# Optimization experiments

Measured on AMD Instinct MI355X. Metric: run time of the kernel, lower is better.

Reference implementation:

```python
import jax, jax.numpy as jnp
import numpy as np

B, T, C, H = 8, 2048, 1024, 128

def setup_inputs() -> dict:
    key = jax.random.key(0)
    kx, kq, kk, kv = jax.random.split(key, 4)
    x = jax.random.normal(kx, (B, T, C), dtype=jnp.float32)
    Wq = jax.random.normal(kq, (C, H), dtype=jnp.float32) * 0.02
    Wk = jax.random.normal(kk, (C, H), dtype=jnp.float32) * 0.02
    Wv = jax.random.normal(kv, (C, H), dtype=jnp.float32) * 0.02
    return {"x": x, "Wq": Wq, "Wk": Wk, "Wv": Wv}

def reference(x, Wq, Wk, Wv):
    # q,k,v: [B,T,H] via bias-free dense projections
    q = jnp.einsum('btc,ch->bth', x, Wq)
    k = jnp.einsum('btc,ch->bth', x, Wk)
    v = jnp.einsum('btc,ch->bth', x, Wv)
    scale = k.shape[-1] ** (-0.5)
    # scores: [B,T,T]
    wei = jnp.einsum('bth,bsh->bts', q, k) * scale
    Tlen = x.shape[1]
    causal = jnp.tril(jnp.ones((Tlen, Tlen), dtype=bool))  # True = keep
    wei = jnp.where(causal[None, :, :], wei, -jnp.inf)
    wei = jax.nn.softmax(wei, axis=-1)
    return jnp.einsum('bts,bsh->bth', wei, v)
```

## Files before the change

### kernel.cpp

```cpp
#include <hip/hip_runtime.h>

#define B_ 8
#define T_ 2048
#define C_ 1024
#define H_ 128
#define BT_ (B_*T_)

typedef unsigned short u16;
typedef unsigned int u32;
typedef __attribute__((ext_vector_type(4))) float f32x4;
typedef __attribute__((ext_vector_type(8))) __bf16 bf16x8;

__device__ __forceinline__ u16 f2bf(float f) {
  u32 u = __float_as_uint(f);
  u += 0x7fffu + ((u >> 16) & 1u);
  return (u16)(u >> 16);
}

#define GLL16(g, l) __builtin_amdgcn_global_load_lds( \
    (const __attribute__((address_space(1))) void*)(g), \
    (__attribute__((address_space(3))) void*)(l), 16, 0, 0)

__device__ __forceinline__ bf16x8 load_frag(const u16* base, int stride, int row0, int k0, int lane) {
  const u16* p = base + (size_t)(row0 + (lane & 15)) * stride + k0 + ((lane >> 4) << 3);
  return *reinterpret_cast<const bf16x8*>(p);
}

__device__ __forceinline__ bf16x8 cvt8n(f32x4 lo, f32x4 hi) {
  bf16x8 r;
#pragma unroll
  for (int i = 0; i < 4; i++) { r[i] = (__bf16)lo[i]; r[4 + i] = (__bf16)hi[i]; }
  return r;
}

__global__ void wt_kernel(const float* __restrict__ Wq, const float* __restrict__ Wk,
                          const float* __restrict__ Wv, u16* __restrict__ wt) {
  int mat = blockIdx.y;
  const float* W = (mat == 0) ? Wq : (mat == 1) ? Wk : Wv;
  int i = blockIdx.x * 256 + threadIdx.x;
  int h = i >> 10;
  int c = i & 1023;
  wt[mat * (C_ * H_) + i] = f2bf(W[c * H_ + h]);
}

__global__ __launch_bounds__(512, 4) void qkv_gemm(const float* __restrict__ x, const u16* __restrict__ wt,
                                                   u16* __restrict__ q, u16* __restrict__ k2,
                                                   u16* __restrict__ vt) {
  __shared__ __align__(16) float As[2][64 * 64];
  __shared__ __align__(16) u16 Bs[2][192 * 64];
  int t = threadIdx.x;
  int lane = t & 63, w = t >> 6;
  int wm = w >> 2, wn = w & 3;
  int quad = lane >> 4, col = lane & 15;
  int m0 = blockIdx.x * 64;
  int nb = blockIdx.y * 192;

  int arow = t >> 4;
  int acg = (t & 15) ^ (arow & 15);
  const float* ax0 = x + (size_t)(m0 + arow) * C_ + acg * 4;
  const float* ax1 = ax0 + (size_t)32 * C_;
  int brow = t >> 3;
  int bcg = (t & 7) ^ (brow & 7);
  const u16* bw0 = wt + (size_t)(nb + brow) * C_ + bcg * 8;
  const u16* bw1 = bw0 + (size_t)64 * C_;
  const u16* bw2 = bw0 + (size_t)128 * C_;

#define STAGE(st, buf) do { \
    int ko_ = (st) * 64; \
    GLL16(ax0 + ko_, &As[buf][t * 4]); \
    GLL16(ax1 + ko_, &As[buf][2048 + t * 4]); \
    GLL16(bw0 + ko_, &Bs[buf][t * 8]); \
    GLL16(bw1 + ko_, &Bs[buf][4096 + t * 8]); \
    GLL16(bw2 + ko_, &Bs[buf][8192 + t * 8]); \
  } while (0)

  STAGE(0, 0);

  f32x4 acc[2][3] = {};
#pragma unroll 2
  for (int kk = 0; kk < 16; kk++) {
    int cur = kk & 1;
    __syncthreads();
    if (kk + 1 < 16) STAGE(kk + 1, cur ^ 1);
    const float* Ab = &As[cur][0];
    const u16* Bb = &Bs[cur][0];
#pragma unroll
    for (int ks = 0; ks < 2; ks++) {
      bf16x8 af[2], bfr[3];
#pragma unroll
      for (int mt = 0; mt < 2; mt++) {
        int rr = wm * 32 + mt * 16 + col;
        int s0 = (ks * 8 + quad * 2) ^ (rr & 15);
        int s1 = s0 ^ 1;
        f32x4 lo = *reinterpret_cast<const f32x4*>(Ab + rr * 64 + s0 * 4);
        f32x4 hi = *reinterpret_cast<const f32x4*>(Ab + rr * 64 + s1 * 4);
        af[mt] = cvt8n(lo, hi);
      }
#pragma unroll
      for (int nt = 0; nt < 3; nt++) {
        int rr = wn * 48 + nt * 16 + col;
        int sl = (ks * 4 + quad) ^ (rr & 7);
        bfr[nt] = *reinterpret_cast<const bf16x8*>(Bb + rr * 64 + sl * 8);
      }
#pragma unroll
      for (int mt = 0; mt < 2; mt++)
#pragma unroll
        for (int nt = 0; nt < 3; nt++)
          acc[mt][nt] = __builtin_amdgcn_mfma_f32_16x16x32_bf16(af[mt], bfr[nt], acc[mt][nt], 0, 0, 0);
    }
  }
#undef STAGE

#pragma unroll
  for (int mt = 0; mt < 2; mt++) {
    int row0 = m0 + wm * 32 + mt * 16 + quad * 4;
#pragma unroll
    for (int nt = 0; nt < 3; nt++) {
      int n = nb + wn * 48 + nt * 16 + col;
      int mat = n >> 7, h = n & 127;
      if (mat == 0) {
#pragma unroll
        for (int r = 0; r < 4; r++) q[(size_t)(row0 + r) * H_ + h] = f2bf(acc[mt][nt][r]);
      } else if (mat == 1) {
#pragma unroll
        for (int r = 0; r < 4; r++) k2[(size_t)(row0 + r) * H_ + h] = f2bf(acc[mt][nt][r]);
      } else {
        int bb = row0 >> 11, tt = row0 & 2047;
        ushort4 pk;
        pk.x = f2bf(acc[mt][nt][0]); pk.y = f2bf(acc[mt][nt][1]);
        pk.z = f2bf(acc[mt][nt][2]); pk.w = f2bf(acc[mt][nt][3]);
        *reinterpret_cast<ushort4*>(&vt[((size_t)bb * H_ + h) * T_ + tt]) = pk;
      }
    }
  }
}

__global__ __launch_bounds__(256) void attn_part(const u16* __restrict__ q, const u16* __restrict__ k,
                                                 const u16* __restrict__ vt,
                                                 float* __restrict__ Op, float* __restrict__ lsum) {
  __shared__ __align__(16) u16 Ks[2][32 * 136];
  __shared__ __align__(16) u16 Vs[2][128 * 40];
  __shared__ __align__(16) u16 P[4][2][16 * 40];
  int t = threadIdx.x;
  int lane = t & 63, w = t >> 6;
  int quad = lane >> 4, col = lane & 15;
  int bx = blockIdx.x;
  int qt = 31 - (bx >> 4);
  int s = (bx >> 3) & 1;
  int b = bx & 7;
  const float scale = 0.08838834764831845f;

  int nk = 2 * (qt + 1);
  int n0 = qt + 1;
  int it0 = s ? n0 : 0;
  int it1 = s ? nk : n0;

  int krow0 = t >> 4, ke = (t & 15) * 8;
  int krow1 = krow0 + 16;
  int vrow0 = t >> 2, ve = (t & 3) * 8;
  int vrow1 = vrow0 + 64;

  int qrow0 = b * T_ + qt * 64 + w * 16;
  bf16x8 qf[4];
#pragma unroll
  for (int ks = 0; ks < 4; ks++) qf[ks] = load_frag(q, H_, qrow0, ks * 32, lane);

  f32x4 o[8] = {};
  float l[4] = {0.f, 0.f, 0.f, 0.f};
  int myqrow = qt * 64 + w * 16 + quad * 4;

  {
    const u16* kb = k + (size_t)(b * T_ + it0 * 32) * H_;
    *reinterpret_cast<uint4*>(&Ks[0][krow0 * 136 + ke]) = *reinterpret_cast<const uint4*>(kb + (size_t)krow0 * 128 + ke);
    *reinterpret_cast<uint4*>(&Ks[0][krow1 * 136 + ke]) = *reinterpret_cast<const uint4*>(kb + (size_t)krow1 * 128 + ke);
    const u16* vb = vt + (size_t)b * H_ * T_ + it0 * 32;
    *reinterpret_cast<uint4*>(&Vs[0][vrow0 * 40 + ve]) = *reinterpret_cast<const uint4*>(vb + (size_t)vrow0 * T_ + ve);
    *reinterpret_cast<uint4*>(&Vs[0][vrow1 * 40 + ve]) = *reinterpret_cast<const uint4*>(vb + (size_t)vrow1 * T_ + ve);
  }

  for (int kt = it0; kt < it1; kt++) {
    int cur = (kt - it0) & 1;
    __syncthreads();
    bool more = (kt + 1 < it1);
    uint4 kc0, kc1, vc0, vc1;
    if (more) {
      const u16* kb = k + (size_t)(b * T_ + (kt + 1) * 32) * H_;
      kc0 = *reinterpret_cast<const uint4*>(kb + (size_t)krow0 * 128 + ke);
      kc1 = *reinterpret_cast<const uint4*>(kb + (size_t)krow1 * 128 + ke);
      const u16* vb = vt + (size_t)b * H_ * T_ + (kt + 1) * 32;
      vc0 = *reinterpret_cast<const uint4*>(vb + (size_t)vrow0 * T_ + ve);
      vc1 = *reinterpret_cast<const uint4*>(vb + (size_t)vrow1 * T_ + ve);
    }

    f32x4 s0 = {}, s1 = {};
#pragma unroll
    for (int ks = 0; ks < 4; ks++) {
      bf16x8 kb0 = *reinterpret_cast<const bf16x8*>(&Ks[cur][col * 136 + ks * 32 + quad * 8]);
      bf16x8 kb1 = *reinterpret_cast<const bf16x8*>(&Ks[cur][(col + 16) * 136 + ks * 32 + quad * 8]);
      s0 = __builtin_amdgcn_mfma_f32_16x16x32_bf16(qf[ks], kb0, s0, 0, 0, 0);
      s1 = __builtin_amdgcn_mfma_f32_16x16x32_bf16(qf[ks], kb1, s1, 0, 0, 0);
    }

    float pv[8];
    int kcol0 = kt * 32 + col;
#pragma unroll
    for (int r = 0; r < 4; r++) {
      int qr = myqrow + r;
      float a0 = fminf(s0[r] * scale, 30.f);
      float a1 = fminf(s1[r] * scale, 30.f);
      a0 = (kcol0      > qr) ? -1e30f : a0;
      a1 = (kcol0 + 16 > qr) ? -1e30f : a1;
      float p0 = __expf(a0);
      float p1 = __expf(a1);
      pv[r] = p0; pv[4 + r] = p1;
      l[r] += p0 + p1;
    }

    u16* Pb = &P[w][cur][0];
#pragma unroll
    for (int r = 0; r < 4; r++) {
      Pb[(quad * 4 + r) * 40 + col] = f2bf(pv[r]);
      Pb[(quad * 4 + r) * 40 + col + 16] = f2bf(pv[4 + r]);
    }
    asm volatile("" ::: "memory");
    __builtin_amdgcn_s_waitcnt(0xc07f);
    asm volatile("" ::: "memory");
    bf16x8 pf = *reinterpret_cast<const bf16x8*>(&Pb[col * 40 + (quad << 3)]);

#pragma unroll
    for (int ht = 0; ht < 8; ht++) {
      bf16x8 vf = *reinterpret_cast<const bf16x8*>(&Vs[cur][(ht * 16 + col) * 40 + quad * 8]);
      o[ht] = __builtin_amdgcn_mfma_f32_16x16x32_bf16(pf, vf, o[ht], 0, 0, 0);
    }

    if (more) {
      int nxt = cur ^ 1;
      *reinterpret_cast<uint4*>(&Ks[nxt][krow0 * 136 + ke]) = kc0;
      *reinterpret_cast<uint4*>(&Ks[nxt][krow1 * 136 + ke]) = kc1;
      *reinterpret_cast<uint4*>(&Vs[nxt][vrow0 * 40 + ve]) = vc0;
      *reinterpret_cast<uint4*>(&Vs[nxt][vrow1 * 40 + ve]) = vc1;
    }
  }

#pragma unroll
  for (int r = 0; r < 4; r++) {
    float v = l[r];
    v += __shfl_xor(v, 1);
    v += __shfl_xor(v, 2);
    v += __shfl_xor(v, 4);
    v += __shfl_xor(v, 8);
    l[r] = v;
  }

  int tile = (s * 8 + b) * 32 + qt;
  float* Orow = Op + (size_t)tile * (64 * 128);
  float* lrow = lsum + (size_t)tile * 64;
  int rowin0 = w * 16 + quad * 4;
  if (col == 0) {
#pragma unroll
    for (int r = 0; r < 4; r++) lrow[rowin0 + r] = l[r];
  }
#pragma unroll
  for (int ht = 0; ht < 8; ht++) {
#pragma unroll
    for (int r = 0; r < 4; r++)
      Orow[(size_t)(rowin0 + r) * 128 + ht * 16 + col] = o[ht][r];
  }
}

__global__ __launch_bounds__(256) void attn_comb(const float* __restrict__ Op, const float* __restrict__ lsum,
                                                 float* __restrict__ out) {
  int bx = blockIdx.x;
  int b = bx >> 5, qt = bx & 31;
  int t = threadIdx.x;
  int h = t & 127, half = t >> 7;
  int tile0 = b * 32 + qt;
  int tile1 = tile0 + 256;
#pragma unroll 4
  for (int rr = 0; rr < 32; rr++) {
    int row = half * 32 + rr;
    float l0 = lsum[tile0 * 64 + row];
    float l1 = lsum[tile1 * 64 + row];
    float rl = 1.f / (l0 + l1);
    float v = (Op[(size_t)tile0 * 8192 + row * 128 + h] +
               Op[(size_t)tile1 * 8192 + row * 128 + h]) * rl;
    out[((size_t)(b * T_ + qt * 64 + row)) * H_ + h] = v;
  }
}

extern "C" void kernel_launch(void* const* d_in, const int* in_sizes, int n_in,
                              void* d_out, int out_size, void* d_ws, size_t ws_size,
                              hipStream_t stream) {
  (void)in_sizes; (void)n_in; (void)out_size; (void)ws_size;
  const float* x  = (const float*)d_in[0];
  const float* Wq = (const float*)d_in[1];
  const float* Wk = (const float*)d_in[2];
  const float* Wv = (const float*)d_in[3];
  u16* ws = (u16*)d_ws;
  u16* q  = ws;
  u16* k  = ws + (size_t)BT_ * H_;
  u16* vt = ws + 2 * (size_t)BT_ * H_;
  u16* wt = ws + 3 * (size_t)BT_ * H_;
  float* Op = (float*)(ws + 3 * (size_t)BT_ * H_ + 3 * C_ * H_);
  float* lsum = Op + (size_t)512 * 64 * 128;
  float* out = (float*)d_out;

  wt_kernel<<<dim3(512, 3), 256, 0, stream>>>(Wq, Wk, Wv, wt);
  qkv_gemm<<<dim3(BT_ / 64, 2), 512, 0, stream>>>(x, wt, q, k, vt);
  attn_part<<<dim3(512), 256, 0, stream>>>(q, k, vt, Op, lsum);
  attn_comb<<<dim3(256), 256, 0, stream>>>(Op, lsum, out);
}
```

Before: 162.3 us.

## Split attention KV range four ways and load K/V fragments directly from global

Attention partial kernel now splits each query tile's key range into four parts instead of two, doubling the grid to 1024 blocks. It drops the LDS double-buffering of K and V and instead loads MFMA fragments straight from global memory (relying on L2/cache), removing the block-wide barriers. The combine kernel now sums four partials. This trades LDS reuse across the four waves for more parallelism and fewer syncs, but each wave now redundantly fetches the same K/V from global memory, and the partial-output traffic doubles.

```diff
diff --git a/kernel.cpp b/kernel.cpp
--- a/kernel.cpp
+++ b/kernel.cpp
@@ -135,74 +135,59 @@
   }
 }
 
-__global__ __launch_bounds__(256) void attn_part(const u16* __restrict__ q, const u16* __restrict__ k,
-                                                 const u16* __restrict__ vt,
-                                                 float* __restrict__ Op, float* __restrict__ lsum) {
-  __shared__ __align__(16) u16 Ks[2][32 * 136];
-  __shared__ __align__(16) u16 Vs[2][128 * 40];
+__global__ __launch_bounds__(256, 4) void attn_part(const u16* __restrict__ q, const u16* __restrict__ k,
+                                                    const u16* __restrict__ vt,
+                                                    float* __restrict__ Op, float* __restrict__ lsum) {
   __shared__ __align__(16) u16 P[4][2][16 * 40];
   int t = threadIdx.x;
   int lane = t & 63, w = t >> 6;
   int quad = lane >> 4, col = lane & 15;
   int bx = blockIdx.x;
-  int qt = 31 - (bx >> 4);
-  int s = (bx >> 3) & 1;
+  int qt = 31 - (bx >> 5);
+  int s = (bx >> 3) & 3;
   int b = bx & 7;
   const float scale = 0.08838834764831845f;
 
   int nk = 2 * (qt + 1);
-  int n0 = qt + 1;
-  int it0 = s ? n0 : 0;
-  int it1 = s ? nk : n0;
-
-  int krow0 = t >> 4, ke = (t & 15) * 8;
-  int krow1 = krow0 + 16;
-  int vrow0 = t >> 2, ve = (t & 3) * 8;
-  int vrow1 = vrow0 + 64;
+  int it0 = (s * nk) >> 2;
+  int it1 = ((s + 1) * nk) >> 2;
 
   int qrow0 = b * T_ + qt * 64 + w * 16;
   bf16x8 qf[4];
 #pragma unroll
   for (int ks = 0; ks < 4; ks++) qf[ks] = load_frag(q, H_, qrow0, ks * 32, lane);
+
+  const u16* kb_b = k + (size_t)b * T_ * H_;
+  const u16* vb_b = vt + (size_t)b * H_ * T_;
 
   f32x4 o[8] = {};
   float l[4] = {0.f, 0.f, 0.f, 0.f};
   int myqrow = qt * 64 + w * 16 + quad * 4;
 
-  {
-    const u16* kb = k + (size_t)(b * T_ + it0 * 32) * H_;
-    *reinterpret_cast<uint4*>(&Ks[0][krow0 * 136 + ke]) = *reinterpret_cast<const uint4*>(kb + (size_t)krow0 * 128 + ke);
-    *reinterpret_cast<uint4*>(&Ks[0][krow1 * 136 + ke]) = *reinterpret_cast<const uint4*>(kb + (size_t)krow1 * 128 + ke);
-    const u16* vb = vt + (size_t)b * H_ * T_ + it0 * 32;
-    *reinterpret_cast<uint4*>(&Vs[0][vrow0 * 40 + ve]) = *reinterpret_cast<const uint4*>(vb + (size_t)vrow0 * T_ + ve);
-    *reinterpret_cast<uint4*>(&Vs[0][vrow1 * 40 + ve]) = *reinterpret_cast<const uint4*>(vb + (size_t)vrow1 * T_ + ve);
-  }
-
+#pragma unroll 2
   for (int kt = it0; kt < it1; kt++) {
     int cur = (kt - it0) & 1;
-    __syncthreads();
-    bool more = (kt + 1 < it1);
-    uint4 kc0, kc1, vc0, vc1;
-    if (more) {
-      const u16* kb = k + (size_t)(b * T_ + (kt + 1) * 32) * H_;
-      kc0 = *reinterpret_cast<const uint4*>(kb + (size_t)krow0 * 128 + ke);
-      kc1 = *reinterpret_cast<const uint4*>(kb + (size_t)krow1 * 128 + ke);
-      const u16* vb = vt + (size_t)b * H_ * T_ + (kt + 1) * 32;
-      vc0 = *reinterpret_cast<const uint4*>(vb + (size_t)vrow0 * T_ + ve);
-      vc1 = *reinterpret_cast<const uint4*>(vb + (size_t)vrow1 * T_ + ve);
-    }
+    int kr0 = kt * 32;
+
+    bf16x8 kf[8], vf[8];
+#pragma unroll
+    for (int ks = 0; ks < 4; ks++) {
+      kf[2 * ks]     = load_frag(kb_b, H_, kr0, ks * 32, lane);
+      kf[2 * ks + 1] = load_frag(kb_b, H_, kr0 + 16, ks * 32, lane);
+    }
+#pragma unroll
+    for (int ht = 0; ht < 8; ht++)
+      vf[ht] = load_frag(vb_b, T_, ht * 16, kr0, lane);
 
     f32x4 s0 = {}, s1 = {};
 #pragma unroll
     for (int ks = 0; ks < 4; ks++) {
-      bf16x8 kb0 = *reinterpret_cast<const bf16x8*>(&Ks[cur][col * 136 + ks * 32 + quad * 8]);
-      bf16x8 kb1 = *reinterpret_cast<const bf16x8*>(&Ks[cur][(col + 16) * 136 + ks * 32 + quad * 8]);
-      s0 = __builtin_amdgcn_mfma_f32_16x16x32_bf16(qf[ks], kb0, s0, 0, 0, 0);
-      s1 = __builtin_amdgcn_mfma_f32_16x16x32_bf16(qf[ks], kb1, s1, 0, 0, 0);
+      s0 = __builtin_amdgcn_mfma_f32_16x16x32_bf16(qf[ks], kf[2 * ks], s0, 0, 0, 0);
+      s1 = __builtin_amdgcn_mfma_f32_16x16x32_bf16(qf[ks], kf[2 * ks + 1], s1, 0, 0, 0);
     }
 
     float pv[8];
-    int kcol0 = kt * 32 + col;
+    int kcol0 = kr0 + col;
 #pragma unroll
     for (int r = 0; r < 4; r++) {
       int qr = myqrow + r;
@@ -228,18 +213,8 @@
     bf16x8 pf = *reinterpret_cast<const bf16x8*>(&Pb[col * 40 + (quad << 3)]);
 
 #pragma unroll
-    for (int ht = 0; ht < 8; ht++) {
-      bf16x8 vf = *reinterpret_cast<const bf16x8*>(&Vs[cur][(ht * 16 + col) * 40 + quad * 8]);
-      o[ht] = __builtin_amdgcn_mfma_f32_16x16x32_bf16(pf, vf, o[ht], 0, 0, 0);
-    }
-
-    if (more) {
-      int nxt = cur ^ 1;
-      *reinterpret_cast<uint4*>(&Ks[nxt][krow0 * 136 + ke]) = kc0;
-      *reinterpret_cast<uint4*>(&Ks[nxt][krow1 * 136 + ke]) = kc1;
-      *reinterpret_cast<uint4*>(&Vs[nxt][vrow0 * 40 + ve]) = vc0;
-      *reinterpret_cast<uint4*>(&Vs[nxt][vrow1 * 40 + ve]) = vc1;
-    }
+    for (int ht = 0; ht < 8; ht++)
+      o[ht] = __builtin_amdgcn_mfma_f32_16x16x32_bf16(pf, vf[ht], o[ht], 0, 0, 0);
   }
 
 #pragma unroll
@@ -275,16 +250,17 @@
   int t = threadIdx.x;
   int h = t & 127, half = t >> 7;
   int tile0 = b * 32 + qt;
-  int tile1 = tile0 + 256;
 #pragma unroll 4
   for (int rr = 0; rr < 32; rr++) {
     int row = half * 32 + rr;
-    float l0 = lsum[tile0 * 64 + row];
-    float l1 = lsum[tile1 * 64 + row];
-    float rl = 1.f / (l0 + l1);
-    float v = (Op[(size_t)tile0 * 8192 + row * 128 + h] +
-               Op[(size_t)tile1 * 8192 + row * 128 + h]) * rl;
-    out[((size_t)(b * T_ + qt * 64 + row)) * H_ + h] = v;
+    float ls = 0.f, v = 0.f;
+#pragma unroll
+    for (int p = 0; p < 4; p++) {
+      int tp = tile0 + p * 256;
+      ls += lsum[tp * 64 + row];
+      v  += Op[(size_t)tp * 8192 + row * 128 + h];
+    }
+    out[((size_t)(b * T_ + qt * 64 + row)) * H_ + h] = v / ls;
   }
 }
 
@@ -302,11 +278,11 @@
   u16* vt = ws + 2 * (size_t)BT_ * H_;
   u16* wt = ws + 3 * (size_t)BT_ * H_;
   float* Op = (float*)(ws + 3 * (size_t)BT_ * H_ + 3 * C_ * H_);
-  float* lsum = Op + (size_t)512 * 64 * 128;
+  float* lsum = Op + (size_t)1024 * 64 * 128;
   float* out = (float*)d_out;
 
   wt_kernel<<<dim3(512, 3), 256, 0, stream>>>(Wq, Wk, Wv, wt);
   qkv_gemm<<<dim3(BT_ / 64, 2), 512, 0, stream>>>(x, wt, q, k, vt);
-  attn_part<<<dim3(512), 256, 0, stream>>>(q, k, vt, Op, lsum);
+  attn_part<<<dim3(1024), 256, 0, stream>>>(q, k, vt, Op, lsum);
   attn_comb<<<dim3(256), 256, 0, stream>>>(Op, lsum, out);
 }
```

New measurement: 201.8 us. 24.3% more time.
